# Kernel tuning notes

Measured on AMD Instinct MI355X. Metric: run time of the kernel, lower is better.

Reference implementation:

```python
import jax, jax.numpy as jnp
import numpy as np

D = 64        # symbol_repr_size
NCLS = 10     # n_classes; embedding row NCLS is the 'inf' token
BSZ = 1024
L = 1024      # power of 2 -> perfect segment tree, tree_len = 2*L - 1


def _rms(t):
    # matches: x / x.pow(2).mean(-1,keepdim=True).add(1e-6).sqrt().add(1e-6)
    return t / (jnp.sqrt(jnp.mean(t * t, axis=-1, keepdims=True) + 1e-6) + 1e-6)


def _gate_combine(left, right, Wr):
    # left,right: [b,n,d]; Wr: [2,d,d] (rule weight reshaped).
    # rule(vec(outer(left,right))) == einsum without materializing [b,n,d,d].
    scores = jnp.einsum('bni,kij,bnj->bnk', left, Wr, right)
    alpha = jax.nn.softmax(scores, axis=-1)                      # [b,n,2]
    return _rms(alpha[..., 0:1] * left + alpha[..., 1:2] * right)


def setup_inputs() -> dict:
    key = jax.random.key(0)
    k = jax.random.split(key, 6)
    x = jax.random.randint(k[0], (BSZ, L), 0, NCLS, dtype=jnp.int32)
    a = jax.random.randint(k[1], (BSZ,), 0, L, dtype=jnp.int32)
    b = jax.random.randint(k[2], (BSZ,), 0, L, dtype=jnp.int32)
    return {
        'x': x,
        'query_low': jnp.minimum(a, b),
        'query_high': jnp.maximum(a, b),
        'embedding': jax.random.normal(k[3], (NCLS + 1, D), jnp.float32),
        'rule_w': jax.random.normal(k[4], (2, D * D), jnp.float32) / D,
        'linear_w': jax.random.normal(k[5], (NCLS, D), jnp.float32) / 8.0,
    }


def reference(x, query_low, query_high, embedding, rule_w, linear_w):
    bsz, l = x.shape
    d = embedding.shape[1]
    Wr = rule_w.reshape(2, d, d)
    inf_tok = embedding[-1]                 # [d], the 'inf' token (row n_classes)

    h = _rms(embedding[x])                  # [b,l,d] leaf symbols

    # ---- build neural segment tree, bottom-up (vectorized per level) ----
    levels = [h]                            # levels[0] = leaves (2^depth nodes)
    cur = h
    while cur.shape[1] > 1:
        cur = _gate_combine(cur[:, 0::2], cur[:, 1::2], Wr)
        levels.append(cur)                  # parents of previous level

    # ---- range min query, bottom-up over all nodes (masked per batch) ----
    res = None
    for nodes in levels:                    # leaves first, root last
        n = nodes.shape[1]
        seg = l // n                        # segment length covered per node
        lows = jnp.arange(n, dtype=query_low.dtype) * seg
        highs = lows + (seg - 1)
        inside = (query_low[:, None] <= lows) & (query_high[:, None] >= highs)
        disjoint = (query_low[:, None] > highs) | (query_high[:, None] < lows)
        if res is None:
            # leaf: either fully inside the query range or disjoint from it
            res = jnp.where(inside[..., None], nodes, inf_tok)
        else:
            comb = _gate_combine(res[:, 0::2], res[:, 1::2], Wr)
            res = jnp.where(inside[..., None], nodes,
                            jnp.where(disjoint[..., None], inf_tok, comb))
    returns = res[:, 0]                     # root answer, [b,d]
    return returns @ linear_w.T             # logits [b, n_classes]
```

## Files before the change

### kernel.cpp

```cpp
#include <hip/hip_runtime.h>

#define NCLS 10

typedef _Float16 half8 __attribute__((ext_vector_type(8)));
typedef _Float16 h2 __attribute__((ext_vector_type(2)));
typedef __fp16 fp16x2 __attribute__((ext_vector_type(2)));
typedef float f32x4 __attribute__((ext_vector_type(4)));
typedef unsigned int u32;

#define MFMA(A, B, C) __builtin_amdgcn_mfma_f32_16x16x32_f16(A, B, C, 0, 0, 0)

union U4H8 { uint4 u; half8 h; h2 p[4]; u32 w[4]; };
union U2H4 { uint2 u; h2 p[2]; };
union HCVT { fp16x2 f; h2 h; u32 w; };

__device__ __forceinline__ int rc(int row, int c) { return (row << 3) | (c ^ (row & 7)); }
__device__ __forceinline__ h2 pk2(float a, float b) { HCVT u; u.f = __builtin_amdgcn_cvt_pkrtz(a, b); return u.h; }
__device__ __forceinline__ u32 packh2(float a, float b) { HCVT u; u.f = __builtin_amdgcn_cvt_pkrtz(a, b); return u.w; }
__device__ __forceinline__ float fdot2f(h2 a, h2 b, float c) { return __builtin_amdgcn_fdot2(a, b, c, false); }
__device__ __forceinline__ float wave_sum(float v) {
#pragma unroll
    for (int m = 1; m < 64; m <<= 1) v += __shfl_xor(v, m, 64);
    return v;
}
__device__ __forceinline__ float red4(float v) {
    v += __shfl_xor(v, 16, 64);
    v += __shfl_xor(v, 32, 64);
    return v;
}

template <int N, bool EXACT>
__device__ __forceinline__ void combine(const uint4* src, const int (&rowL)[N],
                                        const int (&rowR)[N], const half8 (&wfd)[2][4],
                                        int pl, int g, U4H8 (&q)[N][2]) {
    U4H8 La[N][2], Ra[N][2];
#pragma unroll
    for (int n = 0; n < N; ++n)
#pragma unroll
        for (int kb = 0; kb < 2; ++kb) {
            La[n][kb].u = src[rc(rowL[n], g + 4 * kb)];
            Ra[n][kb].u = src[rc(rowR[n], g + 4 * kb)];
        }
    const uint2* s2 = (const uint2*)src;
    U2H4 rv[N][4];
#pragma unroll
    for (int n = 0; n < N; ++n)
#pragma unroll
        for (int mb = 0; mb < 4; ++mb)
            rv[n][mb].u = s2[rc(rowR[n], 2 * mb + (g >> 1)) * 2 + (g & 1)];
    float sd[N], lr[N], ll[N], rr[N];
#pragma unroll
    for (int n = 0; n < N; ++n) { sd[n] = 0.f; lr[n] = 0.f; ll[n] = 0.f; rr[n] = 0.f; }
#pragma unroll
    for (int mb = 0; mb < 4; ++mb)
#pragma unroll
        for (int n = 0; n < N; ++n) {
            f32x4 t = {0.f, 0.f, 0.f, 0.f};
#pragma unroll
            for (int kb = 0; kb < 2; ++kb) t = MFMA(wfd[kb][mb], La[n][kb].h, t);
            sd[n] = fdot2f(pk2(t[0], t[1]), rv[n][mb].p[0],
                           fdot2f(pk2(t[2], t[3]), rv[n][mb].p[1], sd[n]));
        }
#pragma unroll
    for (int n = 0; n < N; ++n)
#pragma unroll
        for (int kb = 0; kb < 2; ++kb)
#pragma unroll
            for (int i = 0; i < 4; ++i) {
                h2 l2 = La[n][kb].p[i], r2 = Ra[n][kb].p[i];
                lr[n] = fdot2f(l2, r2, lr[n]);
                if (EXACT) { ll[n] = fdot2f(l2, l2, ll[n]); rr[n] = fdot2f(r2, r2, rr[n]); }
            }
#pragma unroll
    for (int n = 0; n < N; ++n) {
        sd[n] = red4(sd[n]); lr[n] = red4(lr[n]);
        if (EXACT) { ll[n] = red4(ll[n]); rr[n] = red4(rr[n]); }
    }
#pragma unroll
    for (int n = 0; n < N; ++n) {
        float u = __expf(sd[n]);
        float a0 = __builtin_amdgcn_rcpf(1.f + u), a1 = 1.f - a0;
        float ms = EXACT ? (a0 * a0 * ll[n] + 2.f * a0 * a1 * lr[n] + a1 * a1 * rr[n]) * (1.f / 64.f)
                         : a0 * a0 + a1 * a1 + a0 * a1 * lr[n] * (2.f / 64.f);
        float sc = __builtin_amdgcn_rcpf(__builtin_amdgcn_sqrtf(ms + 1e-6f) + 1e-6f);
        h2 c0 = pk2(a0 * sc, a0 * sc), c1 = pk2(a1 * sc, a1 * sc);
#pragma unroll
        for (int kb = 0; kb < 2; ++kb)
#pragma unroll
            for (int i = 0; i < 4; ++i)
                q[n][kb].p[i] = c0 * La[n][kb].p[i] + c1 * Ra[n][kb].p[i];
    }
}

__device__ __forceinline__ void load_wfd(const uint4* ws4, half8 (&wfd)[2][4], int lane) {
#pragma unroll
    for (int fm = 0; fm < 8; ++fm) {
        U4H8 t;
        t.u = ws4[fm * 64 + lane];
        wfd[fm >> 2][fm & 3] = t.h;
    }
}

__global__ void setup_kernel(const float* __restrict__ emb,
                             const float* __restrict__ rule_w, uint4* __restrict__ ws4) {
    int tid = threadIdx.x;
    int idx = blockIdx.x * 256 + tid;
    {
        int e2 = idx & 3, lane = (idx >> 2) & 63, fm = idx >> 8;
        int kb = fm >> 2, mb = fm & 3, pl = lane & 15, g = lane >> 4;
        int i0 = 32 * kb + 8 * g + 2 * e2, j = 16 * mb + pl;
        float d0 = rule_w[4096 + i0 * 64 + j] - rule_w[i0 * 64 + j];
        float d1 = rule_w[4096 + (i0 + 1) * 64 + j] - rule_w[(i0 + 1) * 64 + j];
        ((u32*)ws4)[idx] = packh2(d0, d1);
    }
    if (blockIdx.x == 0 && tid < 64) {
        int lane = tid;
        u32* eg = (u32*)(ws4 + 512);
        for (int r = 0; r < 11; ++r) {
            float e = emb[r * 64 + lane];
            float ms = wave_sum(e * e) * (1.f / 64.f);
            float v = e * __builtin_amdgcn_rcpf(__builtin_amdgcn_sqrtf(ms + 1e-6f) + 1e-6f);
            u32 w = packh2(v, __shfl_xor(v, 1, 64));
            if ((lane & 1) == 0) eg[r * 32 + (lane >> 1)] = w;
        }
        float e = emb[640 + lane];
        u32 w = packh2(e, __shfl_xor(e, 1, 64));
        if ((lane & 1) == 0) eg[11 * 32 + (lane >> 1)] = w;
    }
}

__global__ void __launch_bounds__(64, 4) fold_kernel(
    const int* __restrict__ x, uint4* __restrict__ ws4) {
    __shared__ uint4 trs[(64 + 12) * 8];
    const int lane = threadIdx.x;
    const int pl = lane & 15, g = lane >> 4;
    const int b = blockIdx.x >> 3, s = blockIdx.x & 7;

    half8 wfd[2][4];
    load_wfd(ws4, wfd, lane);
    {
        int r = lane >> 3, c = lane & 7;
        trs[rc(64 + r, c)] = ws4[512 + lane];
        int idx = lane + 64;
        if (idx < 96) { r = idx >> 3; c = idx & 7; trs[rc(64 + r, c)] = ws4[512 + idx]; }
    }
    const int2* x2 = (const int2*)x;
    int2 c00 = x2[b * 512 + s * 64 + pl];
    int2 c01 = x2[b * 512 + s * 64 + 16 + pl];
    int2 c10 = x2[b * 512 + s * 64 + 32 + pl];
    int2 c11 = x2[b * 512 + s * 64 + 48 + pl];
    asm volatile("s_waitcnt lgkmcnt(0) vmcnt(0)" ::: "memory");

    U4H8 q[2][2];
    {
        int rL[2] = {64 + c00.x, 64 + c01.x}, rR[2] = {64 + c00.y, 64 + c01.y};
        combine<2, false>(trs, rL, rR, wfd, pl, g, q);
        trs[rc(pl, g)] = q[0][0].u;      trs[rc(pl, g + 4)] = q[0][1].u;
        trs[rc(16 + pl, g)] = q[1][0].u; trs[rc(16 + pl, g + 4)] = q[1][1].u;
    }
    {
        int rL[2] = {64 + c10.x, 64 + c11.x}, rR[2] = {64 + c10.y, 64 + c11.y};
        combine<2, false>(trs, rL, rR, wfd, pl, g, q);
        trs[rc(32 + pl, g)] = q[0][0].u; trs[rc(32 + pl, g + 4)] = q[0][1].u;
        trs[rc(48 + pl, g)] = q[1][0].u; trs[rc(48 + pl, g + 4)] = q[1][1].u;
    }
    asm volatile("s_waitcnt lgkmcnt(0)" ::: "memory");
    {
        int rL[2] = {2 * pl, 32 + 2 * pl}, rR[2] = {2 * pl + 1, 33 + 2 * pl};
        combine<2, false>(trs, rL, rR, wfd, pl, g, q);
        trs[rc(pl, g)] = q[0][0].u;      trs[rc(pl, g + 4)] = q[0][1].u;
        trs[rc(16 + pl, g)] = q[1][0].u; trs[rc(16 + pl, g + 4)] = q[1][1].u;
    }
    asm volatile("s_waitcnt lgkmcnt(0)" ::: "memory");
    {
        int rL[1] = {2 * pl}, rR[1] = {2 * pl + 1};
        U4H8 q1[1][2];
        combine<1, false>(trs, rL, rR, wfd, pl, g, q1);
        long gr = 1024 + (long)(b * 128 + s * 16 + pl) * 8;
        ws4[gr + g] = q1[0][0].u;
        ws4[gr + 4 + g] = q1[0][1].u;
    }
}

__global__ void __launch_bounds__(64, 2) topwalk_kernel(
    const int* __restrict__ x, const int* __restrict__ qlo_p,
    const int* __restrict__ qhi_p, const float* __restrict__ lin_w,
    float* __restrict__ out, const uint4* __restrict__ ws4) {
    __shared__ uint4 scr[196 * 8];
    const int lane = threadIdx.x;
    const int pl = lane & 15, g = lane >> 4;
    const int b = blockIdx.x;
    const int lo = qlo_p[b], hi = qhi_p[b];

    half8 wfd[2][4];
    load_wfd(ws4, wfd, lane);
    {
        int r = lane >> 3, c = lane & 7;
        scr[rc(184 + r, c)] = ws4[512 + lane];
        int idx = lane + 64;
        if (idx < 96) { r = idx >> 3; c = idx & 7; scr[rc(184 + r, c)] = ws4[512 + idx]; }
    }
#pragma unroll
    for (int i = 0; i < 16; ++i) {
        int idx = i * 64 + lane;
        int r = idx >> 3, c = idx & 7;
        scr[rc(r, c)] = ws4[1024 + (long)b * 1024 + idx];
    }
    asm volatile("s_waitcnt lgkmcnt(0) vmcnt(0)" ::: "memory");
    if (lane < 32) {
        int slot = lane >> 3, c = lane & 7;
        int il3 = lo >> 3, ih3 = hi >> 3;
        int t3 = (slot == 0) ? il3 : (slot == 1) ? (il3 ^ 1) : (slot == 2) ? ih3 : (ih3 ^ 1);
        scr[rc(140 + slot, c)] = scr[rc(t3, c)];
        int t0 = (slot == 0) ? lo : (slot == 1) ? (lo ^ 1) : (slot == 2) ? hi : (hi ^ 1);
        int cls = x[b * 1024 + t0];
        scr[rc(128 + slot, c)] = scr[rc(184 + cls, c)];
    }
    asm volatile("s_waitcnt lgkmcnt(0) vmcnt(0)" ::: "memory");

    auto capl = [&](int lev, int node, const U4H8 (&qq)[2]) {
        int il = lo >> lev, ih = hi >> lev, cnt = 1024 >> lev;
        int svb = 128 + lev * 4;
        if (node == il) { scr[rc(svb, g)] = qq[0].u; scr[rc(svb, g + 4)] = qq[1].u; }
        if (((il ^ 1) < cnt) && node == (il ^ 1)) { scr[rc(svb + 1, g)] = qq[0].u; scr[rc(svb + 1, g + 4)] = qq[1].u; }
        if (node == ih) { scr[rc(svb + 2, g)] = qq[0].u; scr[rc(svb + 2, g + 4)] = qq[1].u; }
        if (((ih ^ 1) < cnt) && node == (ih ^ 1)) { scr[rc(svb + 3, g)] = qq[0].u; scr[rc(svb + 3, g + 4)] = qq[1].u; }
    };

    U4H8 q[2][2];
    {
        int rL[2] = {2 * pl, 32 + 2 * pl}, rR[2] = {2 * pl + 1, 33 + 2 * pl};
        combine<2, false>(scr, rL, rR, wfd, pl, g, q);
        scr[rc(pl, g)] = q[0][0].u;      scr[rc(pl, g + 4)] = q[0][1].u;
        scr[rc(16 + pl, g)] = q[1][0].u; scr[rc(16 + pl, g + 4)] = q[1][1].u;
        capl(4, pl, q[0]); capl(4, 16 + pl, q[1]);
    }
    {
        int rL[2] = {64 + 2 * pl, 96 + 2 * pl}, rR[2] = {65 + 2 * pl, 97 + 2 * pl};
        combine<2, false>(scr, rL, rR, wfd, pl, g, q);
        scr[rc(32 + pl, g)] = q[0][0].u; scr[rc(32 + pl, g + 4)] = q[0][1].u;
        scr[rc(48 + pl, g)] = q[1][0].u; scr[rc(48 + pl, g + 4)] = q[1][1].u;
        capl(4, 32 + pl, q[0]); capl(4, 48 + pl, q[1]);
    }
    asm volatile("s_waitcnt lgkmcnt(0)" ::: "memory");
    {
        int rL[2] = {2 * pl, 32 + 2 * pl}, rR[2] = {2 * pl + 1, 33 + 2 * pl};
        combine<2, false>(scr, rL, rR, wfd, pl, g, q);
        scr[rc(pl, g)] = q[0][0].u;      scr[rc(pl, g + 4)] = q[0][1].u;
        scr[rc(16 + pl, g)] = q[1][0].u; scr[rc(16 + pl, g + 4)] = q[1][1].u;
        capl(5, pl, q[0]); capl(5, 16 + pl, q[1]);
    }
    asm volatile("s_waitcnt lgkmcnt(0)" ::: "memory");
    const int il1 = lo >> 1, ih1 = hi >> 1, il2 = lo >> 2, ih2 = hi >> 2;
    {
        const int2* x2 = (const int2*)x;
        bool aact = pl < 8;
        int n1 = 0;
        if (aact) {
            int base2 = (pl < 4) ? ((pl < 2) ? il2 : (il2 ^ 1))
                                 : ((pl < 6) ? ih2 : (ih2 ^ 1));
            n1 = 2 * base2 + (pl & 1);
        }
        int2 lv = aact ? x2[b * 512 + n1] : make_int2(0, 0);
        int rL[2] = {2 * pl, aact ? 184 + lv.x : 184};
        int rR[2] = {2 * pl + 1, aact ? 184 + lv.y : 184};
        combine<2, false>(scr, rL, rR, wfd, pl, g, q);
        scr[rc(pl, g)] = q[0][0].u; scr[rc(pl, g + 4)] = q[0][1].u;
        capl(6, pl, q[0]);
        if (aact) { scr[rc(175 + pl, g)] = q[1][0].u; scr[rc(175 + pl, g + 4)] = q[1][1].u; }
    }
    asm volatile("s_waitcnt lgkmcnt(0)" ::: "memory");
    if (lane < 32) {
        int slot = lane >> 3, c = lane & 7;
        int srcrow = (slot == 0) ? 175 + (il1 & 1)
                   : (slot == 1) ? 175 + ((il1 & 1) ^ 1)
                   : (slot == 2) ? 179 + (ih1 & 1)
                                 : 179 + ((ih1 & 1) ^ 1);
        scr[rc(132 + slot, c)] = scr[rc(srcrow, c)];
    }
    asm volatile("s_waitcnt lgkmcnt(0)" ::: "memory");

    int cur_lo = 128, cur_hi = 130;
#pragma unroll 1
    for (int wl = 1; wl <= 10; ++wl) {
        int il = lo >> wl, ih = hi >> wl;
        int ilc = lo >> (wl - 1), ihc = hi >> (wl - 1);
        auto child_row = [&](int c) -> int {
            if (c == ilc) return cur_lo;
            if (c == ihc) return cur_hi;
            int clow = c << (wl - 1);
            int chigh = clow + (1 << (wl - 1)) - 1;
            if (lo <= clow && hi >= chigh)
                return 128 + (wl - 1) * 4 + ((c == (ilc ^ 1)) ? 1 : 3);
            return 195;
        };
        int np = (wl <= 4) ? (16 >> wl) : 0;
        int rowL, rowR, dst;
        bool wm = true, istree = false;
        if (pl < np)       { rowL = 2 * pl; rowR = 2 * pl + 1; dst = pl; istree = true; }
        else if (wl == 1 && pl >= 8 && pl < 12) {
            int s2 = pl - 8; rowL = 175 + 2 * s2; rowR = 176 + 2 * s2; dst = 136 + s2;
        }
        else if (pl == 14) { rowL = child_row(2 * il); rowR = child_row(2 * il + 1); dst = 173; }
        else if (pl == 15) { rowL = child_row(2 * ih); rowR = child_row(2 * ih + 1); dst = 174; }
        else               { rowL = 195; rowR = 195; dst = 175; wm = false; }
        int rLa[1] = {rowL}, rRa[1] = {rowR};
        U4H8 q1[1][2];
        combine<1, true>(scr, rLa, rRa, wfd, pl, g, q1);
        if (wm) { scr[rc(dst, g)] = q1[0][0].u; scr[rc(dst, g + 4)] = q1[0][1].u; }
        if (istree) capl(wl + 6, pl, q1[0]);
        int low = il << wl, high = low + (1 << wl) - 1;
        cur_lo = (lo <= low && hi >= high) ? (128 + wl * 4) : 173;
        int low2 = ih << wl, high2 = low2 + (1 << wl) - 1;
        cur_hi = (lo <= low2 && hi >= high2) ? (128 + wl * 4 + 2) : 174;
        asm volatile("s_waitcnt lgkmcnt(0)" ::: "memory");
    }
    float rv = (float)((_Float16*)scr)[rc(cur_lo, lane >> 3) * 8 + (lane & 7)];
#pragma unroll
    for (int c = 0; c < NCLS; ++c) {
        float s = wave_sum(rv * lin_w[c * 64 + lane]);
        if (lane == 0) out[b * NCLS + c] = s;
    }
}

extern "C" void kernel_launch(void* const* d_in, const int* in_sizes, int n_in,
                              void* d_out, int out_size, void* d_ws, size_t ws_size,
                              hipStream_t stream) {
    const int* x = (const int*)d_in[0];
    const int* qlo = (const int*)d_in[1];
    const int* qhi = (const int*)d_in[2];
    const float* emb = (const float*)d_in[3];
    const float* rule_w = (const float*)d_in[4];
    const float* lin_w = (const float*)d_in[5];
    float* out = (float*)d_out;
    uint4* ws4 = (uint4*)d_ws;
    setup_kernel<<<8, 256, 0, stream>>>(emb, rule_w, ws4);
    fold_kernel<<<8192, 64, 0, stream>>>(x, ws4);
    topwalk_kernel<<<1024, 64, 0, stream>>>(x, qlo, qhi, lin_w, out, ws4);
}
```

Baseline: 54.65 us.

## Keep subtree fold results in registers across levels, writing only right children to LDS

Each lane now owns a contiguous run of 4 (or 8) nodes, so the left and right fragments for the next levels stay in registers. Only right children are written to LDS, because the scalar rv slice still needs a differently permuted layout. This cuts LDS stores and loads and some waitcnt stalls in both the fold and topwalk kernels. It also lowers topwalk launch bounds to one block per CU to allow more registers, at some occupancy risk.

```diff
diff --git a/kernel.cpp b/kernel.cpp
--- a/kernel.cpp
+++ b/kernel.cpp
@@ -30,24 +30,9 @@
 }
 
 template <int N, bool EXACT>
-__device__ __forceinline__ void combine(const uint4* src, const int (&rowL)[N],
-                                        const int (&rowR)[N], const half8 (&wfd)[2][4],
-                                        int pl, int g, U4H8 (&q)[N][2]) {
-    U4H8 La[N][2], Ra[N][2];
-#pragma unroll
-    for (int n = 0; n < N; ++n)
-#pragma unroll
-        for (int kb = 0; kb < 2; ++kb) {
-            La[n][kb].u = src[rc(rowL[n], g + 4 * kb)];
-            Ra[n][kb].u = src[rc(rowR[n], g + 4 * kb)];
-        }
-    const uint2* s2 = (const uint2*)src;
-    U2H4 rv[N][4];
-#pragma unroll
-    for (int n = 0; n < N; ++n)
-#pragma unroll
-        for (int mb = 0; mb < 4; ++mb)
-            rv[n][mb].u = s2[rc(rowR[n], 2 * mb + (g >> 1)) * 2 + (g & 1)];
+__device__ __forceinline__ void combine_core(const U4H8 (&La)[N][2], const U4H8 (&Ra)[N][2],
+                                             const U2H4 (&rv)[N][4], const half8 (&wfd)[2][4],
+                                             U4H8 (&q)[N][2]) {
     float sd[N], lr[N], ll[N], rr[N];
 #pragma unroll
     for (int n = 0; n < N; ++n) { sd[n] = 0.f; lr[n] = 0.f; ll[n] = 0.f; rr[n] = 0.f; }
@@ -90,6 +75,31 @@
             for (int i = 0; i < 4; ++i)
                 q[n][kb].p[i] = c0 * La[n][kb].p[i] + c1 * Ra[n][kb].p[i];
     }
+}
+
+__device__ __forceinline__ void load_bfrag(const uint4* src, int row, int g, U4H8 (&A)[2]) {
+    A[0].u = src[rc(row, g)];
+    A[1].u = src[rc(row, g + 4)];
+}
+__device__ __forceinline__ void load_rv4(const uint4* src, int row, int g, U2H4 (&rv)[4]) {
+    const uint2* s2 = (const uint2*)src;
+#pragma unroll
+    for (int mb = 0; mb < 4; ++mb) rv[mb].u = s2[rc(row, 2 * mb + (g >> 1)) * 2 + (g & 1)];
+}
+
+template <int N, bool EXACT>
+__device__ __forceinline__ void combine_lds(const uint4* src, const int (&rowL)[N],
+                                            const int (&rowR)[N], const half8 (&wfd)[2][4],
+                                            int pl, int g, U4H8 (&q)[N][2]) {
+    U4H8 La[N][2], Ra[N][2];
+    U2H4 rv[N][4];
+#pragma unroll
+    for (int n = 0; n < N; ++n) {
+        load_bfrag(src, rowL[n], g, La[n]);
+        load_bfrag(src, rowR[n], g, Ra[n]);
+        load_rv4(src, rowR[n], g, rv[n]);
+    }
+    combine_core<N, EXACT>(La, Ra, rv, wfd, q);
 }
 
 __device__ __forceinline__ void load_wfd(const uint4* ws4, half8 (&wfd)[2][4], int lane) {
@@ -145,44 +155,66 @@
         if (idx < 96) { r = idx >> 3; c = idx & 7; trs[rc(64 + r, c)] = ws4[512 + idx]; }
     }
     const int2* x2 = (const int2*)x;
-    int2 c00 = x2[b * 512 + s * 64 + pl];
-    int2 c01 = x2[b * 512 + s * 64 + 16 + pl];
-    int2 c10 = x2[b * 512 + s * 64 + 32 + pl];
-    int2 c11 = x2[b * 512 + s * 64 + 48 + pl];
+    int2 cx[4];
+#pragma unroll
+    for (int k = 0; k < 4; ++k) cx[k] = x2[b * 512 + s * 64 + 4 * pl + k];
     asm volatile("s_waitcnt lgkmcnt(0) vmcnt(0)" ::: "memory");
 
-    U4H8 q[2][2];
-    {
-        int rL[2] = {64 + c00.x, 64 + c01.x}, rR[2] = {64 + c00.y, 64 + c01.y};
-        combine<2, false>(trs, rL, rR, wfd, pl, g, q);
-        trs[rc(pl, g)] = q[0][0].u;      trs[rc(pl, g + 4)] = q[0][1].u;
-        trs[rc(16 + pl, g)] = q[1][0].u; trs[rc(16 + pl, g + 4)] = q[1][1].u;
-    }
-    {
-        int rL[2] = {64 + c10.x, 64 + c11.x}, rR[2] = {64 + c10.y, 64 + c11.y};
-        combine<2, false>(trs, rL, rR, wfd, pl, g, q);
-        trs[rc(32 + pl, g)] = q[0][0].u; trs[rc(32 + pl, g + 4)] = q[0][1].u;
-        trs[rc(48 + pl, g)] = q[1][0].u; trs[rc(48 + pl, g + 4)] = q[1][1].u;
-    }
-    asm volatile("s_waitcnt lgkmcnt(0)" ::: "memory");
-    {
-        int rL[2] = {2 * pl, 32 + 2 * pl}, rR[2] = {2 * pl + 1, 33 + 2 * pl};
-        combine<2, false>(trs, rL, rR, wfd, pl, g, q);
-        trs[rc(pl, g)] = q[0][0].u;      trs[rc(pl, g + 4)] = q[0][1].u;
-        trs[rc(16 + pl, g)] = q[1][0].u; trs[rc(16 + pl, g + 4)] = q[1][1].u;
-    }
-    asm volatile("s_waitcnt lgkmcnt(0)" ::: "memory");
-    {
-        int rL[1] = {2 * pl}, rR[1] = {2 * pl + 1};
-        U4H8 q1[1][2];
-        combine<1, false>(trs, rL, rR, wfd, pl, g, q1);
+    U4H8 n1[4][2];
+    {
+        U4H8 La[2][2], Ra[2][2], qq[2][2];
+        U2H4 rv[2][4];
+        load_bfrag(trs, 64 + cx[0].x, g, La[0]);
+        load_bfrag(trs, 64 + cx[0].y, g, Ra[0]);
+        load_rv4(trs, 64 + cx[0].y, g, rv[0]);
+        load_bfrag(trs, 64 + cx[1].x, g, La[1]);
+        load_bfrag(trs, 64 + cx[1].y, g, Ra[1]);
+        load_rv4(trs, 64 + cx[1].y, g, rv[1]);
+        combine_core<2, false>(La, Ra, rv, wfd, qq);
+        n1[0][0] = qq[0][0]; n1[0][1] = qq[0][1];
+        n1[1][0] = qq[1][0]; n1[1][1] = qq[1][1];
+        load_bfrag(trs, 64 + cx[2].x, g, La[0]);
+        load_bfrag(trs, 64 + cx[2].y, g, Ra[0]);
+        load_rv4(trs, 64 + cx[2].y, g, rv[0]);
+        load_bfrag(trs, 64 + cx[3].x, g, La[1]);
+        load_bfrag(trs, 64 + cx[3].y, g, Ra[1]);
+        load_rv4(trs, 64 + cx[3].y, g, rv[1]);
+        combine_core<2, false>(La, Ra, rv, wfd, qq);
+        n1[2][0] = qq[0][0]; n1[2][1] = qq[0][1];
+        n1[3][0] = qq[1][0]; n1[3][1] = qq[1][1];
+    }
+    asm volatile("s_waitcnt lgkmcnt(0)" ::: "memory");
+    trs[rc(4 * pl + 1, g)] = n1[1][0].u; trs[rc(4 * pl + 1, g + 4)] = n1[1][1].u;
+    trs[rc(4 * pl + 3, g)] = n1[3][0].u; trs[rc(4 * pl + 3, g + 4)] = n1[3][1].u;
+    asm volatile("s_waitcnt lgkmcnt(0)" ::: "memory");
+
+    U4H8 n2[2][2];
+    {
+        U4H8 La[2][2] = {{n1[0][0], n1[0][1]}, {n1[2][0], n1[2][1]}};
+        U4H8 Ra[2][2] = {{n1[1][0], n1[1][1]}, {n1[3][0], n1[3][1]}};
+        U2H4 rv[2][4];
+        load_rv4(trs, 4 * pl + 1, g, rv[0]);
+        load_rv4(trs, 4 * pl + 3, g, rv[1]);
+        combine_core<2, false>(La, Ra, rv, wfd, n2);
+    }
+    asm volatile("s_waitcnt lgkmcnt(0)" ::: "memory");
+    trs[rc(2 * pl + 1, g)] = n2[1][0].u; trs[rc(2 * pl + 1, g + 4)] = n2[1][1].u;
+    asm volatile("s_waitcnt lgkmcnt(0)" ::: "memory");
+
+    {
+        U4H8 La[1][2] = {{n2[0][0], n2[0][1]}};
+        U4H8 Ra[1][2] = {{n2[1][0], n2[1][1]}};
+        U2H4 rv[1][4];
+        load_rv4(trs, 2 * pl + 1, g, rv[0]);
+        U4H8 q3[1][2];
+        combine_core<1, false>(La, Ra, rv, wfd, q3);
         long gr = 1024 + (long)(b * 128 + s * 16 + pl) * 8;
-        ws4[gr + g] = q1[0][0].u;
-        ws4[gr + 4 + g] = q1[0][1].u;
-    }
-}
-
-__global__ void __launch_bounds__(64, 2) topwalk_kernel(
+        ws4[gr + g] = q3[0][0].u;
+        ws4[gr + 4 + g] = q3[0][1].u;
+    }
+}
+
+__global__ void __launch_bounds__(64, 1) topwalk_kernel(
     const int* __restrict__ x, const int* __restrict__ qlo_p,
     const int* __restrict__ qhi_p, const float* __restrict__ lin_w,
     float* __restrict__ out, const uint4* __restrict__ ws4) {
@@ -227,47 +259,75 @@
         if (((ih ^ 1) < cnt) && node == (ih ^ 1)) { scr[rc(svb + 3, g)] = qq[0].u; scr[rc(svb + 3, g + 4)] = qq[1].u; }
     };
 
-    U4H8 q[2][2];
-    {
-        int rL[2] = {2 * pl, 32 + 2 * pl}, rR[2] = {2 * pl + 1, 33 + 2 * pl};
-        combine<2, false>(scr, rL, rR, wfd, pl, g, q);
-        scr[rc(pl, g)] = q[0][0].u;      scr[rc(pl, g + 4)] = q[0][1].u;
-        scr[rc(16 + pl, g)] = q[1][0].u; scr[rc(16 + pl, g + 4)] = q[1][1].u;
-        capl(4, pl, q[0]); capl(4, 16 + pl, q[1]);
-    }
-    {
-        int rL[2] = {64 + 2 * pl, 96 + 2 * pl}, rR[2] = {65 + 2 * pl, 97 + 2 * pl};
-        combine<2, false>(scr, rL, rR, wfd, pl, g, q);
-        scr[rc(32 + pl, g)] = q[0][0].u; scr[rc(32 + pl, g + 4)] = q[0][1].u;
-        scr[rc(48 + pl, g)] = q[1][0].u; scr[rc(48 + pl, g + 4)] = q[1][1].u;
-        capl(4, 32 + pl, q[0]); capl(4, 48 + pl, q[1]);
-    }
-    asm volatile("s_waitcnt lgkmcnt(0)" ::: "memory");
-    {
-        int rL[2] = {2 * pl, 32 + 2 * pl}, rR[2] = {2 * pl + 1, 33 + 2 * pl};
-        combine<2, false>(scr, rL, rR, wfd, pl, g, q);
-        scr[rc(pl, g)] = q[0][0].u;      scr[rc(pl, g + 4)] = q[0][1].u;
-        scr[rc(16 + pl, g)] = q[1][0].u; scr[rc(16 + pl, g + 4)] = q[1][1].u;
-        capl(5, pl, q[0]); capl(5, 16 + pl, q[1]);
-    }
-    asm volatile("s_waitcnt lgkmcnt(0)" ::: "memory");
+    U4H8 n4[4][2];
+    {
+        U4H8 La[2][2], Ra[2][2], qq[2][2];
+        U2H4 rv[2][4];
+        load_bfrag(scr, 8 * pl + 0, g, La[0]);
+        load_bfrag(scr, 8 * pl + 1, g, Ra[0]);
+        load_rv4(scr, 8 * pl + 1, g, rv[0]);
+        load_bfrag(scr, 8 * pl + 2, g, La[1]);
+        load_bfrag(scr, 8 * pl + 3, g, Ra[1]);
+        load_rv4(scr, 8 * pl + 3, g, rv[1]);
+        combine_core<2, false>(La, Ra, rv, wfd, qq);
+        n4[0][0] = qq[0][0]; n4[0][1] = qq[0][1];
+        n4[1][0] = qq[1][0]; n4[1][1] = qq[1][1];
+        load_bfrag(scr, 8 * pl + 4, g, La[0]);
+        load_bfrag(scr, 8 * pl + 5, g, Ra[0]);
+        load_rv4(scr, 8 * pl + 5, g, rv[0]);
+        load_bfrag(scr, 8 * pl + 6, g, La[1]);
+        load_bfrag(scr, 8 * pl + 7, g, Ra[1]);
+        load_rv4(scr, 8 * pl + 7, g, rv[1]);
+        combine_core<2, false>(La, Ra, rv, wfd, qq);
+        n4[2][0] = qq[0][0]; n4[2][1] = qq[0][1];
+        n4[3][0] = qq[1][0]; n4[3][1] = qq[1][1];
+    }
+    asm volatile("s_waitcnt lgkmcnt(0)" ::: "memory");
+    trsW4: ;
+    scr[rc(4 * pl + 1, g)] = n4[1][0].u; scr[rc(4 * pl + 1, g + 4)] = n4[1][1].u;
+    scr[rc(4 * pl + 3, g)] = n4[3][0].u; scr[rc(4 * pl + 3, g + 4)] = n4[3][1].u;
+    capl(4, 4 * pl + 0, n4[0]); capl(4, 4 * pl + 1, n4[1]);
+    capl(4, 4 * pl + 2, n4[2]); capl(4, 4 * pl + 3, n4[3]);
+    asm volatile("s_waitcnt lgkmcnt(0)" ::: "memory");
+
+    U4H8 n5[2][2];
+    {
+        U4H8 La[2][2] = {{n4[0][0], n4[0][1]}, {n4[2][0], n4[2][1]}};
+        U4H8 Ra[2][2] = {{n4[1][0], n4[1][1]}, {n4[3][0], n4[3][1]}};
+        U2H4 rv[2][4];
+        load_rv4(scr, 4 * pl + 1, g, rv[0]);
+        load_rv4(scr, 4 * pl + 3, g, rv[1]);
+        combine_core<2, false>(La, Ra, rv, wfd, n5);
+    }
+    asm volatile("s_waitcnt lgkmcnt(0)" ::: "memory");
+    scr[rc(2 * pl + 1, g)] = n5[1][0].u; scr[rc(2 * pl + 1, g + 4)] = n5[1][1].u;
+    capl(5, 2 * pl, n5[0]); capl(5, 2 * pl + 1, n5[1]);
+    asm volatile("s_waitcnt lgkmcnt(0)" ::: "memory");
+
     const int il1 = lo >> 1, ih1 = hi >> 1, il2 = lo >> 2, ih2 = hi >> 2;
     {
         const int2* x2 = (const int2*)x;
         bool aact = pl < 8;
-        int n1 = 0;
+        int nn1 = 0;
         if (aact) {
             int base2 = (pl < 4) ? ((pl < 2) ? il2 : (il2 ^ 1))
                                  : ((pl < 6) ? ih2 : (ih2 ^ 1));
-            n1 = 2 * base2 + (pl & 1);
+            nn1 = 2 * base2 + (pl & 1);
         }
-        int2 lv = aact ? x2[b * 512 + n1] : make_int2(0, 0);
-        int rL[2] = {2 * pl, aact ? 184 + lv.x : 184};
-        int rR[2] = {2 * pl + 1, aact ? 184 + lv.y : 184};
-        combine<2, false>(scr, rL, rR, wfd, pl, g, q);
-        scr[rc(pl, g)] = q[0][0].u; scr[rc(pl, g + 4)] = q[0][1].u;
-        capl(6, pl, q[0]);
-        if (aact) { scr[rc(175 + pl, g)] = q[1][0].u; scr[rc(175 + pl, g + 4)] = q[1][1].u; }
+        int2 lv = aact ? x2[b * 512 + nn1] : make_int2(0, 0);
+        U4H8 La[2][2], Ra[2][2], qq[2][2];
+        U2H4 rv[2][4];
+        La[0][0] = n5[0][0]; La[0][1] = n5[0][1];
+        Ra[0][0] = n5[1][0]; Ra[0][1] = n5[1][1];
+        load_rv4(scr, 2 * pl + 1, g, rv[0]);
+        load_bfrag(scr, 184 + lv.x, g, La[1]);
+        load_bfrag(scr, 184 + lv.y, g, Ra[1]);
+        load_rv4(scr, 184 + lv.y, g, rv[1]);
+        combine_core<2, false>(La, Ra, rv, wfd, qq);
+        asm volatile("s_waitcnt lgkmcnt(0)" ::: "memory");
+        scr[rc(pl, g)] = qq[0][0].u; scr[rc(pl, g + 4)] = qq[0][1].u;
+        capl(6, pl, qq[0]);
+        if (aact) { scr[rc(175 + pl, g)] = qq[1][0].u; scr[rc(175 + pl, g + 4)] = qq[1][1].u; }
     }
     asm volatile("s_waitcnt lgkmcnt(0)" ::: "memory");
     if (lane < 32) {
@@ -306,7 +366,7 @@
         else               { rowL = 195; rowR = 195; dst = 175; wm = false; }
         int rLa[1] = {rowL}, rRa[1] = {rowR};
         U4H8 q1[1][2];
-        combine<1, true>(scr, rLa, rRa, wfd, pl, g, q1);
+        combine_lds<1, true>(scr, rLa, rRa, wfd, pl, g, q1);
         if (wm) { scr[rc(dst, g)] = q1[0][0].u; scr[rc(dst, g + 4)] = q1[0][1].u; }
         if (istree) capl(wl + 6, pl, q1[0]);
         int low = il << wl, high = low + (1 << wl) - 1;
```

Result: slower. 56.28 us (+3.0%).
